# Kernel optimization log

Hardware: AMD Instinct MI355X
Metric: run time of the kernel (lower is better)

The kernel has to match this reference:

```python
import jax, jax.numpy as jnp
import numpy as np

LR = 0.1
N_HEADS = 4


def setup_inputs() -> dict:
    key = jax.random.key(0)
    ks = jax.random.split(key, 12)
    B, S, D, M, H = 2, 1024, 128, 512, 512
    s = 0.05
    return {
        "x": jax.random.normal(ks[0], (B, S, D), jnp.float32),
        "memory": jax.random.normal(ks[1], (M, D), jnp.float32) * s,
        "w_q": jax.random.normal(ks[2], (D, D), jnp.float32) * s,
        "w_k": jax.random.normal(ks[3], (D, D), jnp.float32) * s,
        "w_v": jax.random.normal(ks[4], (D, D), jnp.float32) * s,
        "b_q": jax.random.normal(ks[5], (D,), jnp.float32) * s,
        "b_k": jax.random.normal(ks[6], (D,), jnp.float32) * s,
        "b_v": jax.random.normal(ks[7], (D,), jnp.float32) * s,
        "w_o": jax.random.normal(ks[8], (D, D), jnp.float32) * s,
        "b_o": jax.random.normal(ks[9], (D,), jnp.float32) * s,
        "w_fc": jax.random.normal(ks[10], (H, D), jnp.float32) * s,
        "b_fc": jax.random.normal(ks[11], (H,), jnp.float32) * s,
    }


def reference(x, memory, w_q, w_k, w_v, b_q, b_k, b_v, w_o, b_o, w_fc, b_fc):
    B, S, D = x.shape
    M = memory.shape[0]
    hd = D // N_HEADS

    # --- LongTermMemory update (broadcast pairwise diff [B,S,M,D]) ---
    diff = x[:, :, None, :] - memory[None, None, :, :]          # [B,S,M,D]
    surprise = jnp.sqrt(jnp.sum(diff * diff, axis=-1, keepdims=True))  # [B,S,M,1]
    agg = jnp.mean(LR * surprise * diff, axis=(0, 1))           # [M,D]
    # torch does memory.data += agg (detached in-place update)
    mem = memory + jax.lax.stop_gradient(agg)                    # [M,D]

    # --- MultiheadAttention(query=x, key=mem, value=mem), batch_first ---
    # mem is identical across batch, so project once.
    q = (x @ w_q.T + b_q).reshape(B, S, N_HEADS, hd)
    k = (mem @ w_k.T + b_k).reshape(M, N_HEADS, hd)
    v = (mem @ w_v.T + b_v).reshape(M, N_HEADS, hd)
    scores = jnp.einsum('bshd,mhd->bhsm', q, k) / jnp.sqrt(jnp.asarray(hd, x.dtype))
    attn = jax.nn.softmax(scores, axis=-1)
    ctx = jnp.einsum('bhsm,mhd->bshd', attn, v).reshape(B, S, D)
    attn_out = ctx @ w_o.T + b_o                                 # [B,S,D]

    # --- Linear + ReLU ---
    return jax.nn.relu(attn_out @ w_fc.T + b_fc)                 # [B,S,hidden]
```

## Files before the change

### kernel.cpp

```cpp
#include <hip/hip_runtime.h>
#include <hip/hip_bf16.h>
#include <math.h>

#define SS 1024
#define MM 512
#define LRC (0.1f/2048.0f)
#define SCALE 0.17677669529663687f

typedef __attribute__((ext_vector_type(8))) short s8v;
typedef __attribute__((ext_vector_type(4))) float f32x4;
#define MFMA16(a, b, c) __builtin_amdgcn_mfma_f32_16x16x32_bf16(a, b, c, 0, 0, 0)

__device__ __forceinline__ unsigned short f2b(float f) {
  union { float f; unsigned int u; } v; v.f = f;
  return (unsigned short)((v.u + 0x7FFFu + ((v.u >> 16) & 1u)) >> 16);
}

__global__ __launch_bounds__(256) void k_prep(
    const float* __restrict__ x, const float* __restrict__ mem,
    const float* __restrict__ wq, const float* __restrict__ wk,
    const float* __restrict__ wv, const float* __restrict__ wo,
    const float* __restrict__ wfc,
    unsigned short* __restrict__ xbf, unsigned short* __restrict__ xT,
    float* __restrict__ xnorm, unsigned short* __restrict__ membf,
    float* __restrict__ mnorm,
    unsigned short* __restrict__ wqb, unsigned short* __restrict__ wkb,
    unsigned short* __restrict__ wvb, unsigned short* __restrict__ wob,
    unsigned short* __restrict__ wfcb) {
  const int t = threadIdx.x, bx = blockIdx.x;
  __shared__ float xl[64][132];
  if (bx < 32) {
    const int r0 = bx * 64;
    for (int i = t; i < 2048; i += 256) {
      int r = i >> 5, c4 = (i & 31) * 4;
      float4 v = *reinterpret_cast<const float4*>(&x[(r0 + r) * 128 + c4]);
      xl[r][c4] = v.x; xl[r][c4+1] = v.y; xl[r][c4+2] = v.z; xl[r][c4+3] = v.w;
      ushort4 u; u.x = f2b(v.x); u.y = f2b(v.y); u.z = f2b(v.z); u.w = f2b(v.w);
      *reinterpret_cast<ushort4*>(&xbf[(r0 + r) * 128 + c4]) = u;
    }
    __syncthreads();
    {
      int r = t >> 2, q = t & 3;
      float s = 0.f;
      #pragma unroll
      for (int j = 0; j < 32; ++j) { float v = xl[r][q * 32 + j]; s += v * v; }
      s += __shfl_xor(s, 1); s += __shfl_xor(s, 2);
      if (q == 0) xnorm[r0 + r] = s;
    }
    {
      int d = t >> 1, hh = t & 1;
      #pragma unroll
      for (int j4 = 0; j4 < 32; j4 += 4) {
        ushort4 u;
        u.x = f2b(xl[hh*32 + j4    ][d]);
        u.y = f2b(xl[hh*32 + j4 + 1][d]);
        u.z = f2b(xl[hh*32 + j4 + 2][d]);
        u.w = f2b(xl[hh*32 + j4 + 3][d]);
        *reinterpret_cast<ushort4*>(&xT[d * 2048 + r0 + hh*32 + j4]) = u;
      }
    }
  } else if (bx < 40) {
    const int r0 = (bx - 32) * 64;
    for (int i = t; i < 2048; i += 256) {
      int r = i >> 5, c4 = (i & 31) * 4;
      float4 v = *reinterpret_cast<const float4*>(&mem[(r0 + r) * 128 + c4]);
      xl[r][c4] = v.x; xl[r][c4+1] = v.y; xl[r][c4+2] = v.z; xl[r][c4+3] = v.w;
      ushort4 u; u.x = f2b(v.x); u.y = f2b(v.y); u.z = f2b(v.z); u.w = f2b(v.w);
      *reinterpret_cast<ushort4*>(&membf[(r0 + r) * 128 + c4]) = u;
    }
    __syncthreads();
    int r = t >> 2, q = t & 3;
    float s = 0.f;
    #pragma unroll
    for (int j = 0; j < 32; ++j) { float v = xl[r][q * 32 + j]; s += v * v; }
    s += __shfl_xor(s, 1); s += __shfl_xor(s, 2);
    if (q == 0) mnorm[r0 + r] = s;
  } else {
    const float* src; unsigned short* dst; int off = 0;
    if (bx == 40)      { src = wq;  dst = wqb; }
    else if (bx == 41) { src = wk;  dst = wkb; }
    else if (bx == 42) { src = wv;  dst = wvb; }
    else if (bx == 43) { src = wo;  dst = wob; }
    else               { src = wfc; dst = wfcb; off = (bx - 44) * 16384; }
    for (int i = t; i < 4096; i += 256) {
      float4 v = *reinterpret_cast<const float4*>(&src[off + i * 4]);
      ushort4 u; u.x = f2b(v.x); u.y = f2b(v.y); u.z = f2b(v.z); u.w = f2b(v.w);
      *reinterpret_cast<ushort4*>(&dst[off + i * 4]) = u;
    }
  }
}

__global__ __launch_bounds__(256) void k_surp(
    const unsigned short* __restrict__ xbf, const unsigned short* __restrict__ membf,
    const float* __restrict__ xnorm, const float* __restrict__ mnorm,
    unsigned short* __restrict__ STb) {
  const int t = threadIdx.x;
  const int bs0 = blockIdx.x * 64, m0 = blockIdx.y * 64;
  const int w = t >> 6, l = t & 63;
  const int kq = (l >> 4) * 8;
  const int arow = bs0 + w * 16 + (l & 15);
  f32x4 acc[4] = {};
  #pragma unroll
  for (int kc = 0; kc < 4; ++kc) {
    s8v a = *reinterpret_cast<const s8v*>(&xbf[arow * 128 + kc * 32 + kq]);
    #pragma unroll
    for (int mt = 0; mt < 4; ++mt) {
      s8v b = *reinterpret_cast<const s8v*>(&membf[(m0 + mt*16 + (l&15)) * 128 + kc*32 + kq]);
      acc[mt] = MFMA16(a, b, acc[mt]);
    }
  }
  const int r0 = bs0 + w * 16 + (l >> 4) * 4;
  float xn[4];
  #pragma unroll
  for (int i = 0; i < 4; ++i) xn[i] = xnorm[r0 + i];
  #pragma unroll
  for (int mt = 0; mt < 4; ++mt) {
    const int col = m0 + mt * 16 + (l & 15);
    const float mn = mnorm[col];
    ushort4 u;
    u.x = f2b(sqrtf(fmaxf(0.f, xn[0] + mn - 2.f * acc[mt][0])));
    u.y = f2b(sqrtf(fmaxf(0.f, xn[1] + mn - 2.f * acc[mt][1])));
    u.z = f2b(sqrtf(fmaxf(0.f, xn[2] + mn - 2.f * acc[mt][2])));
    u.w = f2b(sqrtf(fmaxf(0.f, xn[3] + mn - 2.f * acc[mt][3])));
    *reinterpret_cast<ushort4*>(&STb[col * 2048 + r0]) = u;
  }
}

__global__ __launch_bounds__(256) void k_qkv(
    const unsigned short* __restrict__ xbf, const unsigned short* __restrict__ STb,
    const unsigned short* __restrict__ xT, const float* __restrict__ mem,
    const unsigned short* __restrict__ wqb, const unsigned short* __restrict__ wkb,
    const unsigned short* __restrict__ wvb,
    const float* __restrict__ bq, const float* __restrict__ bk,
    const float* __restrict__ bv,
    unsigned short* __restrict__ qbf, unsigned short* __restrict__ kbf,
    unsigned short* __restrict__ vT) {
  __shared__ float Tld[16][132];
  __shared__ float srowl[16];
  __shared__ unsigned short mnl[16][136];
  const int t = threadIdx.x, bx = blockIdx.x;
  const int w = t >> 6, l = t & 63;
  const int kq = (l >> 4) * 8;
  const int r0l = (l >> 4) * 4;
  if (bx < 32) {
    const int s0 = bx * 64;
    const int arow = s0 + w * 16 + (l & 15);
    f32x4 acc[8] = {};
    #pragma unroll
    for (int kc = 0; kc < 4; ++kc) {
      s8v a = *reinterpret_cast<const s8v*>(&xbf[arow * 128 + kc * 32 + kq]);
      #pragma unroll
      for (int nt = 0; nt < 8; ++nt) {
        s8v b = *reinterpret_cast<const s8v*>(&wqb[(nt*16 + (l&15)) * 128 + kc*32 + kq]);
        acc[nt] = MFMA16(a, b, acc[nt]);
      }
    }
    const int r0 = s0 + w * 16 + r0l;
    #pragma unroll
    for (int nt = 0; nt < 8; ++nt) {
      const int col = nt * 16 + (l & 15);
      const float bb = bq[col];
      #pragma unroll
      for (int i = 0; i < 4; ++i)
        qbf[(r0 + i) * 128 + col] = f2b((acc[nt][i] + bb) * SCALE);
    }
  } else {
    const bool isv = bx >= 64;
    const int m0 = (isv ? (bx - 64) : (bx - 32)) * 16;
    f32x4 acc[2] = {};
    float ssum = 0.f;
    const int arow = m0 + (l & 15);
    #pragma unroll 4
    for (int kk = 0; kk < 64; ++kk) {
      s8v a = *reinterpret_cast<const s8v*>(&STb[arow * 2048 + kk * 32 + kq]);
      #pragma unroll
      for (int j = 0; j < 8; ++j) {
        union { unsigned int u; float f; } cv;
        cv.u = ((unsigned int)(unsigned short)a[j]) << 16;
        ssum += cv.f;
      }
      #pragma unroll
      for (int nt = 0; nt < 2; ++nt) {
        s8v b = *reinterpret_cast<const s8v*>(&xT[(w*32 + nt*16 + (l&15)) * 2048 + kk*32 + kq]);
        acc[nt] = MFMA16(a, b, acc[nt]);
      }
    }
    ssum += __shfl_xor(ssum, 16); ssum += __shfl_xor(ssum, 32);
    if (w == 0 && l < 16) srowl[l] = ssum;
    #pragma unroll
    for (int nt = 0; nt < 2; ++nt) {
      const int col = w * 32 + nt * 16 + (l & 15);
      #pragma unroll
      for (int i = 0; i < 4; ++i) Tld[r0l + i][col] = acc[nt][i];
    }
    __syncthreads();
    #pragma unroll
    for (int i = 0; i < 8; ++i) {
      const int flat = t + 256 * i;
      const int r = flat >> 7, c = flat & 127;
      const float mv = mem[(m0 + r) * 128 + c];
      mnl[r][c] = f2b(mv + LRC * (Tld[r][c] - srowl[r] * mv));
    }
    __syncthreads();
    const unsigned short* W = isv ? wvb : wkb;
    const float* bias = isv ? bv : bk;
    f32x4 pacc[2] = {};
    #pragma unroll
    for (int kc = 0; kc < 4; ++kc) {
      s8v a = *reinterpret_cast<const s8v*>(&mnl[l & 15][kc * 32 + kq]);
      #pragma unroll
      for (int nt = 0; nt < 2; ++nt) {
        s8v b = *reinterpret_cast<const s8v*>(&W[(w*32 + nt*16 + (l&15)) * 128 + kc*32 + kq]);
        pacc[nt] = MFMA16(a, b, pacc[nt]);
      }
    }
    #pragma unroll
    for (int nt = 0; nt < 2; ++nt) {
      const int col = w * 32 + nt * 16 + (l & 15);
      const float bb = bias[col];
      if (!isv) {
        #pragma unroll
        for (int i = 0; i < 4; ++i)
          kbf[(m0 + r0l + i) * 128 + col] = f2b(pacc[nt][i] + bb);
      } else {
        ushort4 u;
        u.x = f2b(pacc[nt][0] + bb); u.y = f2b(pacc[nt][1] + bb);
        u.z = f2b(pacc[nt][2] + bb); u.w = f2b(pacc[nt][3] + bb);
        *reinterpret_cast<ushort4*>(&vT[col * 512 + m0 + r0l]) = u;
      }
    }
  }
}

__global__ __launch_bounds__(256) void k_scores(
    const unsigned short* __restrict__ qbf, const unsigned short* __restrict__ kbf,
    unsigned short* __restrict__ P) {
  const int t = threadIdx.x;
  const int sB = blockIdx.x * 64;
  const int bh = blockIdx.y;
  const int b = bh >> 2, h = bh & 3;
  const int w = t >> 6, l = t & 63;
  const int kq = (l >> 4) * 8;
  const int arow = b * SS + sB + w * 16 + (l & 15);
  const s8v a = *reinterpret_cast<const s8v*>(&qbf[arow * 128 + h * 32 + kq]);
  f32x4 acc[32];
  #pragma unroll
  for (int mt = 0; mt < 32; ++mt) acc[mt] = f32x4{0.f, 0.f, 0.f, 0.f};
  #pragma unroll
  for (int mt = 0; mt < 32; ++mt) {
    s8v b2 = *reinterpret_cast<const s8v*>(&kbf[(mt*16 + (l&15)) * 128 + h*32 + kq]);
    acc[mt] = MFMA16(a, b2, acc[mt]);
  }
  const int prow0 = bh * SS + sB + w * 16 + (l >> 4) * 4;
  #pragma unroll
  for (int i = 0; i < 4; ++i) {
    float mx = acc[0][i];
    #pragma unroll
    for (int mt = 1; mt < 32; ++mt) mx = fmaxf(mx, acc[mt][i]);
    mx = fmaxf(mx, __shfl_xor(mx, 1));
    mx = fmaxf(mx, __shfl_xor(mx, 2));
    mx = fmaxf(mx, __shfl_xor(mx, 4));
    mx = fmaxf(mx, __shfl_xor(mx, 8));
    float sm = 0.f;
    #pragma unroll
    for (int mt = 0; mt < 32; ++mt) {
      float e = __expf(acc[mt][i] - mx); acc[mt][i] = e; sm += e;
    }
    sm += __shfl_xor(sm, 1); sm += __shfl_xor(sm, 2);
    sm += __shfl_xor(sm, 4); sm += __shfl_xor(sm, 8);
    const float inv = 1.f / sm;
    #pragma unroll
    for (int mt = 0; mt < 32; ++mt)
      P[(prow0 + i) * 512 + mt * 16 + (l & 15)] = f2b(acc[mt][i] * inv);
  }
}

__global__ __launch_bounds__(256) void k_pv(
    const unsigned short* __restrict__ P, const unsigned short* __restrict__ vT,
    unsigned short* __restrict__ ctx) {
  const int t = threadIdx.x;
  const int sB = blockIdx.x * 64;
  const int bh = blockIdx.y;
  const int b = bh >> 2, h = bh & 3;
  const int w = t >> 6, l = t & 63;
  const int kq = (l >> 4) * 8;
  const int arow = bh * SS + sB + w * 16 + (l & 15);
  f32x4 acc[2] = {};
  #pragma unroll 4
  for (int kk = 0; kk < 16; ++kk) {
    s8v a = *reinterpret_cast<const s8v*>(&P[arow * 512 + kk * 32 + kq]);
    #pragma unroll
    for (int nt = 0; nt < 2; ++nt) {
      s8v b2 = *reinterpret_cast<const s8v*>(&vT[(h*32 + nt*16 + (l&15)) * 512 + kk*32 + kq]);
      acc[nt] = MFMA16(a, b2, acc[nt]);
    }
  }
  const int r0 = b * SS + sB + w * 16 + (l >> 4) * 4;
  #pragma unroll
  for (int nt = 0; nt < 2; ++nt) {
    const int col = h * 32 + nt * 16 + (l & 15);
    #pragma unroll
    for (int i = 0; i < 4; ++i)
      ctx[(r0 + i) * 128 + col] = f2b(acc[nt][i]);
  }
}

__global__ __launch_bounds__(256) void k_wofc(
    const unsigned short* __restrict__ ctx, const unsigned short* __restrict__ wob,
    const float* __restrict__ bo, const unsigned short* __restrict__ wfcb,
    const float* __restrict__ bfc, float* __restrict__ out) {
  __shared__ unsigned short al[32][136];
  const int t = threadIdx.x;
  const int rows0 = blockIdx.x * 32;
  const int w = t >> 6, l = t & 63;
  const int rt = w >> 1, ch = w & 1;
  const int kq = (l >> 4) * 8;
  {
    const int arow = rows0 + rt * 16 + (l & 15);
    f32x4 acc[4] = {};
    #pragma unroll
    for (int kc = 0; kc < 4; ++kc) {
      s8v a = *reinterpret_cast<const s8v*>(&ctx[arow * 128 + kc * 32 + kq]);
      #pragma unroll
      for (int nt = 0; nt < 4; ++nt) {
        s8v b2 = *reinterpret_cast<const s8v*>(&wob[(ch*64 + nt*16 + (l&15)) * 128 + kc*32 + kq]);
        acc[nt] = MFMA16(a, b2, acc[nt]);
      }
    }
    const int rl0 = rt * 16 + (l >> 4) * 4;
    #pragma unroll
    for (int nt = 0; nt < 4; ++nt) {
      const int col = ch * 64 + nt * 16 + (l & 15);
      const float bb = bo[col];
      #pragma unroll
      for (int i = 0; i < 4; ++i) al[rl0 + i][col] = f2b(acc[nt][i] + bb);
    }
  }
  __syncthreads();
  {
    f32x4 acc[16] = {};
    #pragma unroll
    for (int kc = 0; kc < 4; ++kc) {
      s8v a = *reinterpret_cast<const s8v*>(&al[rt * 16 + (l & 15)][kc * 32 + kq]);
      #pragma unroll
      for (int nt = 0; nt < 16; ++nt) {
        s8v b2 = *reinterpret_cast<const s8v*>(&wfcb[(ch*256 + nt*16 + (l&15)) * 128 + kc*32 + kq]);
        acc[nt] = MFMA16(a, b2, acc[nt]);
      }
    }
    const int r0 = rows0 + rt * 16 + (l >> 4) * 4;
    #pragma unroll
    for (int nt = 0; nt < 16; ++nt) {
      const int col = ch * 256 + nt * 16 + (l & 15);
      const float bb = bfc[col];
      #pragma unroll
      for (int i = 0; i < 4; ++i)
        out[(r0 + i) * 512 + col] = fmaxf(acc[nt][i] + bb, 0.f);
    }
  }
}

extern "C" void kernel_launch(void* const* d_in, const int* in_sizes, int n_in,
                              void* d_out, int out_size, void* d_ws, size_t ws_size,
                              hipStream_t stream) {
  const float* x    = (const float*)d_in[0];
  const float* mem  = (const float*)d_in[1];
  const float* w_q  = (const float*)d_in[2];
  const float* w_k  = (const float*)d_in[3];
  const float* w_v  = (const float*)d_in[4];
  const float* b_q  = (const float*)d_in[5];
  const float* b_k  = (const float*)d_in[6];
  const float* b_v  = (const float*)d_in[7];
  const float* w_o  = (const float*)d_in[8];
  const float* b_o  = (const float*)d_in[9];
  const float* w_fc = (const float*)d_in[10];
  const float* b_fc = (const float*)d_in[11];
  float* out = (float*)d_out;

  char* base = (char*)d_ws;
  unsigned short* P     = (unsigned short*)(base);
  unsigned short* STb   = (unsigned short*)(base + 8388608);
  unsigned short* xbf   = (unsigned short*)(base + 10485760);
  unsigned short* xT    = (unsigned short*)(base + 11010048);
  unsigned short* qbf   = (unsigned short*)(base + 11534336);
  unsigned short* ctx   = (unsigned short*)(base + 12058624);
  unsigned short* kbf   = (unsigned short*)(base + 12582912);
  unsigned short* vT    = (unsigned short*)(base + 12713984);
  unsigned short* membf = (unsigned short*)(base + 12845056);
  unsigned short* wfcb  = (unsigned short*)(base + 12976128);
  unsigned short* wqb   = (unsigned short*)(base + 13107200);
  unsigned short* wkb   = (unsigned short*)(base + 13139968);
  unsigned short* wvb   = (unsigned short*)(base + 13172736);
  unsigned short* wob   = (unsigned short*)(base + 13205504);
  float* xnorm          = (float*)(base + 13238272);
  float* mnorm          = (float*)(base + 13246464);

  k_prep<<<48, 256, 0, stream>>>(x, mem, w_q, w_k, w_v, w_o, w_fc,
                                 xbf, xT, xnorm, membf, mnorm,
                                 wqb, wkb, wvb, wob, wfcb);
  k_surp<<<dim3(32, 8), 256, 0, stream>>>(xbf, membf, xnorm, mnorm, STb);
  k_qkv<<<96, 256, 0, stream>>>(xbf, STb, xT, mem, wqb, wkb, wvb,
                                b_q, b_k, b_v, qbf, kbf, vT);
  k_scores<<<dim3(16, 8), 256, 0, stream>>>(qbf, kbf, P);
  k_pv<<<dim3(16, 8), 256, 0, stream>>>(P, vT, ctx);
  k_wofc<<<64, 256, 0, stream>>>(ctx, wob, b_o, wfcb, b_fc, out);
}
```

Baseline: 72.31 us.

## Fuse six kernels into three: prep+surprise+Q, K/V update, attention+output MLP

Merges prep, surprise distance and Q projection into one kernel whose blocks each convert their own x and memory tiles in shared memory. K and V projections now share one block per memory row tile instead of two. Scores, softmax, PV, output projection and FC run in one kernel, with the probability matrix and context kept in shared memory rather than written to and re-read from global memory. This removes three launches and large intermediate global buffers, at the cost of redundant conversions of x and memory per block and fewer blocks (32) in the K/V stage.

```diff
diff --git a/kernel.cpp b/kernel.cpp
--- a/kernel.cpp
+++ b/kernel.cpp
@@ -16,194 +16,204 @@
   return (unsigned short)((v.u + 0x7FFFu + ((v.u >> 16) & 1u)) >> 16);
 }
 
-__global__ __launch_bounds__(256) void k_prep(
+__global__ __launch_bounds__(256) void k_p1(
     const float* __restrict__ x, const float* __restrict__ mem,
     const float* __restrict__ wq, const float* __restrict__ wk,
     const float* __restrict__ wv, const float* __restrict__ wo,
-    const float* __restrict__ wfc,
-    unsigned short* __restrict__ xbf, unsigned short* __restrict__ xT,
-    float* __restrict__ xnorm, unsigned short* __restrict__ membf,
-    float* __restrict__ mnorm,
-    unsigned short* __restrict__ wqb, unsigned short* __restrict__ wkb,
-    unsigned short* __restrict__ wvb, unsigned short* __restrict__ wob,
-    unsigned short* __restrict__ wfcb) {
-  const int t = threadIdx.x, bx = blockIdx.x;
-  __shared__ float xl[64][132];
-  if (bx < 32) {
-    const int r0 = bx * 64;
-    for (int i = t; i < 2048; i += 256) {
-      int r = i >> 5, c4 = (i & 31) * 4;
-      float4 v = *reinterpret_cast<const float4*>(&x[(r0 + r) * 128 + c4]);
-      xl[r][c4] = v.x; xl[r][c4+1] = v.y; xl[r][c4+2] = v.z; xl[r][c4+3] = v.w;
-      ushort4 u; u.x = f2b(v.x); u.y = f2b(v.y); u.z = f2b(v.z); u.w = f2b(v.w);
-      *reinterpret_cast<ushort4*>(&xbf[(r0 + r) * 128 + c4]) = u;
-    }
-    __syncthreads();
-    {
-      int r = t >> 2, q = t & 3;
-      float s = 0.f;
-      #pragma unroll
-      for (int j = 0; j < 32; ++j) { float v = xl[r][q * 32 + j]; s += v * v; }
-      s += __shfl_xor(s, 1); s += __shfl_xor(s, 2);
-      if (q == 0) xnorm[r0 + r] = s;
-    }
-    {
-      int d = t >> 1, hh = t & 1;
-      #pragma unroll
-      for (int j4 = 0; j4 < 32; j4 += 4) {
-        ushort4 u;
-        u.x = f2b(xl[hh*32 + j4    ][d]);
-        u.y = f2b(xl[hh*32 + j4 + 1][d]);
-        u.z = f2b(xl[hh*32 + j4 + 2][d]);
-        u.w = f2b(xl[hh*32 + j4 + 3][d]);
-        *reinterpret_cast<ushort4*>(&xT[d * 2048 + r0 + hh*32 + j4]) = u;
-      }
-    }
-  } else if (bx < 40) {
-    const int r0 = (bx - 32) * 64;
-    for (int i = t; i < 2048; i += 256) {
-      int r = i >> 5, c4 = (i & 31) * 4;
-      float4 v = *reinterpret_cast<const float4*>(&mem[(r0 + r) * 128 + c4]);
-      xl[r][c4] = v.x; xl[r][c4+1] = v.y; xl[r][c4+2] = v.z; xl[r][c4+3] = v.w;
-      ushort4 u; u.x = f2b(v.x); u.y = f2b(v.y); u.z = f2b(v.z); u.w = f2b(v.w);
-      *reinterpret_cast<ushort4*>(&membf[(r0 + r) * 128 + c4]) = u;
-    }
-    __syncthreads();
-    int r = t >> 2, q = t & 3;
-    float s = 0.f;
-    #pragma unroll
-    for (int j = 0; j < 32; ++j) { float v = xl[r][q * 32 + j]; s += v * v; }
-    s += __shfl_xor(s, 1); s += __shfl_xor(s, 2);
-    if (q == 0) mnorm[r0 + r] = s;
-  } else {
-    const float* src; unsigned short* dst; int off = 0;
-    if (bx == 40)      { src = wq;  dst = wqb; }
-    else if (bx == 41) { src = wk;  dst = wkb; }
-    else if (bx == 42) { src = wv;  dst = wvb; }
-    else if (bx == 43) { src = wo;  dst = wob; }
-    else               { src = wfc; dst = wfcb; off = (bx - 44) * 16384; }
-    for (int i = t; i < 4096; i += 256) {
-      float4 v = *reinterpret_cast<const float4*>(&src[off + i * 4]);
-      ushort4 u; u.x = f2b(v.x); u.y = f2b(v.y); u.z = f2b(v.z); u.w = f2b(v.w);
-      *reinterpret_cast<ushort4*>(&dst[off + i * 4]) = u;
-    }
-  }
-}
-
-__global__ __launch_bounds__(256) void k_surp(
-    const unsigned short* __restrict__ xbf, const unsigned short* __restrict__ membf,
-    const float* __restrict__ xnorm, const float* __restrict__ mnorm,
-    unsigned short* __restrict__ STb) {
-  const int t = threadIdx.x;
-  const int bs0 = blockIdx.x * 64, m0 = blockIdx.y * 64;
-  const int w = t >> 6, l = t & 63;
-  const int kq = (l >> 4) * 8;
-  const int arow = bs0 + w * 16 + (l & 15);
-  f32x4 acc[4] = {};
-  #pragma unroll
-  for (int kc = 0; kc < 4; ++kc) {
-    s8v a = *reinterpret_cast<const s8v*>(&xbf[arow * 128 + kc * 32 + kq]);
-    #pragma unroll
-    for (int mt = 0; mt < 4; ++mt) {
-      s8v b = *reinterpret_cast<const s8v*>(&membf[(m0 + mt*16 + (l&15)) * 128 + kc*32 + kq]);
-      acc[mt] = MFMA16(a, b, acc[mt]);
-    }
-  }
-  const int r0 = bs0 + w * 16 + (l >> 4) * 4;
-  float xn[4];
-  #pragma unroll
-  for (int i = 0; i < 4; ++i) xn[i] = xnorm[r0 + i];
-  #pragma unroll
-  for (int mt = 0; mt < 4; ++mt) {
-    const int col = m0 + mt * 16 + (l & 15);
-    const float mn = mnorm[col];
-    ushort4 u;
-    u.x = f2b(sqrtf(fmaxf(0.f, xn[0] + mn - 2.f * acc[mt][0])));
-    u.y = f2b(sqrtf(fmaxf(0.f, xn[1] + mn - 2.f * acc[mt][1])));
-    u.z = f2b(sqrtf(fmaxf(0.f, xn[2] + mn - 2.f * acc[mt][2])));
-    u.w = f2b(sqrtf(fmaxf(0.f, xn[3] + mn - 2.f * acc[mt][3])));
-    *reinterpret_cast<ushort4*>(&STb[col * 2048 + r0]) = u;
-  }
-}
-
-__global__ __launch_bounds__(256) void k_qkv(
-    const unsigned short* __restrict__ xbf, const unsigned short* __restrict__ STb,
-    const unsigned short* __restrict__ xT, const float* __restrict__ mem,
-    const unsigned short* __restrict__ wqb, const unsigned short* __restrict__ wkb,
-    const unsigned short* __restrict__ wvb,
-    const float* __restrict__ bq, const float* __restrict__ bk,
-    const float* __restrict__ bv,
-    unsigned short* __restrict__ qbf, unsigned short* __restrict__ kbf,
-    unsigned short* __restrict__ vT) {
-  __shared__ float Tld[16][132];
-  __shared__ float srowl[16];
-  __shared__ unsigned short mnl[16][136];
+    const float* __restrict__ wfc, const float* __restrict__ bq,
+    unsigned short* __restrict__ STb, unsigned short* __restrict__ xT,
+    unsigned short* __restrict__ qbf,
+    unsigned short* __restrict__ wkb, unsigned short* __restrict__ wvb,
+    unsigned short* __restrict__ wob, unsigned short* __restrict__ wfcb) {
+  __shared__ alignas(16) char smem[69376];
   const int t = threadIdx.x, bx = blockIdx.x;
   const int w = t >> 6, l = t & 63;
   const int kq = (l >> 4) * 8;
   const int r0l = (l >> 4) * 4;
-  if (bx < 32) {
-    const int s0 = bx * 64;
-    const int arow = s0 + w * 16 + (l & 15);
+
+  if (bx < 256) {
+    float (*xl)[132]          = reinterpret_cast<float (*)[132]>(smem);
+    unsigned short (*xb)[136] = reinterpret_cast<unsigned short (*)[136]>(smem + 33792);
+    unsigned short (*mb)[136] = reinterpret_cast<unsigned short (*)[136]>(smem + 51200);
+    float* xn                 = reinterpret_cast<float*>(smem + 68608);
+    float* mn                 = reinterpret_cast<float*>(smem + 68864);
+    const int bs0 = (bx & 31) * 64, m0 = (bx >> 5) * 64;
+
+    for (int i = t; i < 2048; i += 256) {
+      int r = i >> 5, c4 = (i & 31) * 4;
+      float4 v = *reinterpret_cast<const float4*>(&x[(bs0 + r) * 128 + c4]);
+      xl[r][c4] = v.x; xl[r][c4+1] = v.y; xl[r][c4+2] = v.z; xl[r][c4+3] = v.w;
+      ushort4 u; u.x = f2b(v.x); u.y = f2b(v.y); u.z = f2b(v.z); u.w = f2b(v.w);
+      *reinterpret_cast<ushort4*>(&xb[r][c4]) = u;
+    }
+    __syncthreads();
+    {
+      int r = t >> 2, q = t & 3;
+      float s = 0.f;
+      #pragma unroll
+      for (int j = 0; j < 32; ++j) { float v = xl[r][q * 32 + j]; s += v * v; }
+      s += __shfl_xor(s, 1); s += __shfl_xor(s, 2);
+      if (q == 0) xn[r] = s;
+    }
+    if ((bx >> 5) == 0) {
+      int d = t >> 1, hh = t & 1;
+      #pragma unroll
+      for (int j4 = 0; j4 < 32; j4 += 4) {
+        ushort4 u;
+        u.x = xb[hh*32 + j4    ][d];
+        u.y = xb[hh*32 + j4 + 1][d];
+        u.z = xb[hh*32 + j4 + 2][d];
+        u.w = xb[hh*32 + j4 + 3][d];
+        *reinterpret_cast<ushort4*>(&xT[d * 2048 + bs0 + hh*32 + j4]) = u;
+      }
+    }
+    __syncthreads();
+    for (int i = t; i < 2048; i += 256) {
+      int r = i >> 5, c4 = (i & 31) * 4;
+      float4 v = *reinterpret_cast<const float4*>(&mem[(m0 + r) * 128 + c4]);
+      xl[r][c4] = v.x; xl[r][c4+1] = v.y; xl[r][c4+2] = v.z; xl[r][c4+3] = v.w;
+      ushort4 u; u.x = f2b(v.x); u.y = f2b(v.y); u.z = f2b(v.z); u.w = f2b(v.w);
+      *reinterpret_cast<ushort4*>(&mb[r][c4]) = u;
+    }
+    __syncthreads();
+    {
+      int r = t >> 2, q = t & 3;
+      float s = 0.f;
+      #pragma unroll
+      for (int j = 0; j < 32; ++j) { float v = xl[r][q * 32 + j]; s += v * v; }
+      s += __shfl_xor(s, 1); s += __shfl_xor(s, 2);
+      if (q == 0) mn[r] = s;
+    }
+    __syncthreads();
+    f32x4 acc[4] = {};
+    #pragma unroll
+    for (int kc = 0; kc < 4; ++kc) {
+      s8v a = *reinterpret_cast<const s8v*>(&xb[w*16 + (l&15)][kc*32 + kq]);
+      #pragma unroll
+      for (int mt = 0; mt < 4; ++mt) {
+        s8v b = *reinterpret_cast<const s8v*>(&mb[mt*16 + (l&15)][kc*32 + kq]);
+        acc[mt] = MFMA16(a, b, acc[mt]);
+      }
+    }
+    const int r0g = bs0 + w * 16 + r0l;
+    float xnr[4];
+    #pragma unroll
+    for (int i = 0; i < 4; ++i) xnr[i] = xn[w*16 + r0l + i];
+    #pragma unroll
+    for (int mt = 0; mt < 4; ++mt) {
+      const int coll = mt * 16 + (l & 15);
+      const float mnv = mn[coll];
+      ushort4 u;
+      u.x = f2b(sqrtf(fmaxf(0.f, xnr[0] + mnv - 2.f * acc[mt][0])));
+      u.y = f2b(sqrtf(fmaxf(0.f, xnr[1] + mnv - 2.f * acc[mt][1])));
+      u.z = f2b(sqrtf(fmaxf(0.f, xnr[2] + mnv - 2.f * acc[mt][2])));
+      u.w = f2b(sqrtf(fmaxf(0.f, xnr[3] + mnv - 2.f * acc[mt][3])));
+      *reinterpret_cast<ushort4*>(&STb[(m0 + coll) * 2048 + r0g]) = u;
+    }
+  } else if (bx < 288) {
+    unsigned short (*xb)[136]  = reinterpret_cast<unsigned short (*)[136]>(smem);
+    unsigned short (*wql)[136] = reinterpret_cast<unsigned short (*)[136]>(smem + 17408);
+    const int s0 = (bx - 256) * 64;
+    for (int i = t; i < 2048; i += 256) {
+      int r = i >> 5, c4 = (i & 31) * 4;
+      float4 v = *reinterpret_cast<const float4*>(&x[(s0 + r) * 128 + c4]);
+      ushort4 u; u.x = f2b(v.x); u.y = f2b(v.y); u.z = f2b(v.z); u.w = f2b(v.w);
+      *reinterpret_cast<ushort4*>(&xb[r][c4]) = u;
+    }
+    for (int i = t; i < 4096; i += 256) {
+      int r = i >> 5, c4 = (i & 31) * 4;
+      float4 v = *reinterpret_cast<const float4*>(&wq[r * 128 + c4]);
+      ushort4 u; u.x = f2b(v.x); u.y = f2b(v.y); u.z = f2b(v.z); u.w = f2b(v.w);
+      *reinterpret_cast<ushort4*>(&wql[r][c4]) = u;
+    }
+    __syncthreads();
     f32x4 acc[8] = {};
     #pragma unroll
     for (int kc = 0; kc < 4; ++kc) {
-      s8v a = *reinterpret_cast<const s8v*>(&xbf[arow * 128 + kc * 32 + kq]);
+      s8v a = *reinterpret_cast<const s8v*>(&xb[w*16 + (l&15)][kc*32 + kq]);
       #pragma unroll
       for (int nt = 0; nt < 8; ++nt) {
-        s8v b = *reinterpret_cast<const s8v*>(&wqb[(nt*16 + (l&15)) * 128 + kc*32 + kq]);
+        s8v b = *reinterpret_cast<const s8v*>(&wql[nt*16 + (l&15)][kc*32 + kq]);
         acc[nt] = MFMA16(a, b, acc[nt]);
       }
     }
-    const int r0 = s0 + w * 16 + r0l;
+    const int r0g = s0 + w * 16 + r0l;
     #pragma unroll
     for (int nt = 0; nt < 8; ++nt) {
       const int col = nt * 16 + (l & 15);
       const float bb = bq[col];
       #pragma unroll
       for (int i = 0; i < 4; ++i)
-        qbf[(r0 + i) * 128 + col] = f2b((acc[nt][i] + bb) * SCALE);
+        qbf[(r0g + i) * 128 + col] = f2b((acc[nt][i] + bb) * SCALE);
     }
   } else {
-    const bool isv = bx >= 64;
-    const int m0 = (isv ? (bx - 64) : (bx - 32)) * 16;
-    f32x4 acc[2] = {};
-    float ssum = 0.f;
-    const int arow = m0 + (l & 15);
-    #pragma unroll 4
-    for (int kk = 0; kk < 64; ++kk) {
-      s8v a = *reinterpret_cast<const s8v*>(&STb[arow * 2048 + kk * 32 + kq]);
-      #pragma unroll
-      for (int j = 0; j < 8; ++j) {
-        union { unsigned int u; float f; } cv;
-        cv.u = ((unsigned int)(unsigned short)a[j]) << 16;
-        ssum += cv.f;
-      }
-      #pragma unroll
-      for (int nt = 0; nt < 2; ++nt) {
-        s8v b = *reinterpret_cast<const s8v*>(&xT[(w*32 + nt*16 + (l&15)) * 2048 + kk*32 + kq]);
-        acc[nt] = MFMA16(a, b, acc[nt]);
-      }
-    }
-    ssum += __shfl_xor(ssum, 16); ssum += __shfl_xor(ssum, 32);
-    if (w == 0 && l < 16) srowl[l] = ssum;
+    const float* src; unsigned short* dst; int off = 0;
+    if (bx == 288)      { src = wk;  dst = wkb; }
+    else if (bx == 289) { src = wv;  dst = wvb; }
+    else if (bx == 290) { src = wo;  dst = wob; }
+    else                { src = wfc; dst = wfcb; off = (bx - 291) * 16384; }
+    for (int i = t; i < 4096; i += 256) {
+      float4 v = *reinterpret_cast<const float4*>(&src[off + i * 4]);
+      ushort4 u; u.x = f2b(v.x); u.y = f2b(v.y); u.z = f2b(v.z); u.w = f2b(v.w);
+      *reinterpret_cast<ushort4*>(&dst[off + i * 4]) = u;
+    }
+  }
+}
+
+__global__ __launch_bounds__(256) void k_p2(
+    const unsigned short* __restrict__ STb, const unsigned short* __restrict__ xT,
+    const float* __restrict__ mem,
+    const unsigned short* __restrict__ wkb, const unsigned short* __restrict__ wvb,
+    const float* __restrict__ bk, const float* __restrict__ bv,
+    unsigned short* __restrict__ kbf, unsigned short* __restrict__ vT) {
+  __shared__ float Tld[16][132];
+  __shared__ float srowl[16];
+  __shared__ unsigned short mnl[16][136];
+  const int t = threadIdx.x;
+  const int w = t >> 6, l = t & 63;
+  const int kq = (l >> 4) * 8;
+  const int r0l = (l >> 4) * 4;
+  const int m0 = blockIdx.x * 16;
+
+  f32x4 acc[2] = {};
+  float ssum = 0.f;
+  const int arow = m0 + (l & 15);
+  #pragma unroll 4
+  for (int kk = 0; kk < 64; ++kk) {
+    s8v a = *reinterpret_cast<const s8v*>(&STb[arow * 2048 + kk * 32 + kq]);
+    #pragma unroll
+    for (int j = 0; j < 8; ++j) {
+      union { unsigned int u; float f; } cv;
+      cv.u = ((unsigned int)(unsigned short)a[j]) << 16;
+      ssum += cv.f;
+    }
     #pragma unroll
     for (int nt = 0; nt < 2; ++nt) {
-      const int col = w * 32 + nt * 16 + (l & 15);
-      #pragma unroll
-      for (int i = 0; i < 4; ++i) Tld[r0l + i][col] = acc[nt][i];
-    }
-    __syncthreads();
-    #pragma unroll
-    for (int i = 0; i < 8; ++i) {
-      const int flat = t + 256 * i;
-      const int r = flat >> 7, c = flat & 127;
-      const float mv = mem[(m0 + r) * 128 + c];
-      mnl[r][c] = f2b(mv + LRC * (Tld[r][c] - srowl[r] * mv));
-    }
-    __syncthreads();
-    const unsigned short* W = isv ? wvb : wkb;
-    const float* bias = isv ? bv : bk;
+      s8v b = *reinterpret_cast<const s8v*>(&xT[(w*32 + nt*16 + (l&15)) * 2048 + kk*32 + kq]);
+      acc[nt] = MFMA16(a, b, acc[nt]);
+    }
+  }
+  ssum += __shfl_xor(ssum, 16); ssum += __shfl_xor(ssum, 32);
+  if (w == 0 && l < 16) srowl[l] = ssum;
+  #pragma unroll
+  for (int nt = 0; nt < 2; ++nt) {
+    const int col = w * 32 + nt * 16 + (l & 15);
+    #pragma unroll
+    for (int i = 0; i < 4; ++i) Tld[r0l + i][col] = acc[nt][i];
+  }
+  __syncthreads();
+  #pragma unroll
+  for (int i = 0; i < 8; ++i) {
+    const int flat = t + 256 * i;
+    const int r = flat >> 7, c = flat & 127;
+    const float mv = mem[(m0 + r) * 128 + c];
+    mnl[r][c] = f2b(mv + LRC * (Tld[r][c] - srowl[r] * mv));
+  }
+  __syncthreads();
+  #pragma unroll
+  for (int p = 0; p < 2; ++p) {
+    const unsigned short* W = p ? wvb : wkb;
+    const float* bias = p ? bv : bk;
     f32x4 pacc[2] = {};
     #pragma unroll
     for (int kc = 0; kc < 4; ++kc) {
@@ -218,7 +228,7 @@
     for (int nt = 0; nt < 2; ++nt) {
       const int col = w * 32 + nt * 16 + (l & 15);
       const float bb = bias[col];
-      if (!isv) {
+      if (p == 0) {
         #pragma unroll
         for (int i = 0; i < 4; ++i)
           kbf[(m0 + r0l + i) * 128 + col] = f2b(pacc[nt][i] + bb);
@@ -232,130 +242,113 @@
   }
 }
 
-__global__ __launch_bounds__(256) void k_scores(
+__global__ __launch_bounds__(256) void k_p3(
     const unsigned short* __restrict__ qbf, const unsigned short* __restrict__ kbf,
-    unsigned short* __restrict__ P) {
+    const unsigned short* __restrict__ vT, const unsigned short* __restrict__ wob,
+    const unsigned short* __restrict__ wfcb, const float* __restrict__ bo,
+    const float* __restrict__ bfc, float* __restrict__ out) {
+  __shared__ alignas(16) char smem[75264];
+  unsigned short (*Pl)[520] = reinterpret_cast<unsigned short (*)[520]>(smem);
+  unsigned short (*cl)[136] = reinterpret_cast<unsigned short (*)[136]>(smem + 66560);
+  unsigned short (*al)[136] = reinterpret_cast<unsigned short (*)[136]>(smem + 70912);
   const int t = threadIdx.x;
-  const int sB = blockIdx.x * 64;
-  const int bh = blockIdx.y;
-  const int b = bh >> 2, h = bh & 3;
   const int w = t >> 6, l = t & 63;
   const int kq = (l >> 4) * 8;
-  const int arow = b * SS + sB + w * 16 + (l & 15);
-  const s8v a = *reinterpret_cast<const s8v*>(&qbf[arow * 128 + h * 32 + kq]);
-  f32x4 acc[32];
-  #pragma unroll
-  for (int mt = 0; mt < 32; ++mt) acc[mt] = f32x4{0.f, 0.f, 0.f, 0.f};
-  #pragma unroll
-  for (int mt = 0; mt < 32; ++mt) {
-    s8v b2 = *reinterpret_cast<const s8v*>(&kbf[(mt*16 + (l&15)) * 128 + h*32 + kq]);
-    acc[mt] = MFMA16(a, b2, acc[mt]);
-  }
-  const int prow0 = bh * SS + sB + w * 16 + (l >> 4) * 4;
-  #pragma unroll
-  for (int i = 0; i < 4; ++i) {
-    float mx = acc[0][i];
-    #pragma unroll
-    for (int mt = 1; mt < 32; ++mt) mx = fmaxf(mx, acc[mt][i]);
-    mx = fmaxf(mx, __shfl_xor(mx, 1));
-    mx = fmaxf(mx, __shfl_xor(mx, 2));
-    mx = fmaxf(mx, __shfl_xor(mx, 4));
-    mx = fmaxf(mx, __shfl_xor(mx, 8));
-    float sm = 0.f;
+  const int r0l = (l >> 4) * 4;
+  const int r0 = blockIdx.x * 16;
+
+  {
+    const int h = w;
+    const s8v a = *reinterpret_cast<const s8v*>(&qbf[(r0 + (l & 15)) * 128 + h * 32 + kq]);
+    f32x4 acc[32];
+    #pragma unroll
+    for (int mt = 0; mt < 32; ++mt) acc[mt] = f32x4{0.f, 0.f, 0.f, 0.f};
     #pragma unroll
     for (int mt = 0; mt < 32; ++mt) {
-      float e = __expf(acc[mt][i] - mx); acc[mt][i] = e; sm += e;
-    }
-    sm += __shfl_xor(sm, 1); sm += __shfl_xor(sm, 2);
-    sm += __shfl_xor(sm, 4); sm += __shfl_xor(sm, 8);
-    const float inv = 1.f / sm;
-    #pragma unroll
-    for (int mt = 0; mt < 32; ++mt)
-      P[(prow0 + i) * 512 + mt * 16 + (l & 15)] = f2b(acc[mt][i] * inv);
-  }
-}
-
-__global__ __launch_bounds__(256) void k_pv(
-    const unsigned short* __restrict__ P, const unsigned short* __restrict__ vT,
-    unsigned short* __restrict__ ctx) {
-  const int t = threadIdx.x;
-  const int sB = blockIdx.x * 64;
-  const int bh = blockIdx.y;
-  const int b = bh >> 2, h = bh & 3;
-  const int w = t >> 6, l = t & 63;
-  const int kq = (l >> 4) * 8;
-  const int arow = bh * SS + sB + w * 16 + (l & 15);
-  f32x4 acc[2] = {};
-  #pragma unroll 4
-  for (int kk = 0; kk < 16; ++kk) {
-    s8v a = *reinterpret_cast<const s8v*>(&P[arow * 512 + kk * 32 + kq]);
+      s8v b2 = *reinterpret_cast<const s8v*>(&kbf[(mt*16 + (l&15)) * 128 + h*32 + kq]);
+      acc[mt] = MFMA16(a, b2, acc[mt]);
+    }
+    #pragma unroll
+    for (int i = 0; i < 4; ++i) {
+      float mx = acc[0][i];
+      #pragma unroll
+      for (int mt = 1; mt < 32; ++mt) mx = fmaxf(mx, acc[mt][i]);
+      mx = fmaxf(mx, __shfl_xor(mx, 1));
+      mx = fmaxf(mx, __shfl_xor(mx, 2));
+      mx = fmaxf(mx, __shfl_xor(mx, 4));
+      mx = fmaxf(mx, __shfl_xor(mx, 8));
+      float sm = 0.f;
+      #pragma unroll
+      for (int mt = 0; mt < 32; ++mt) {
+        float e = __expf(acc[mt][i] - mx); acc[mt][i] = e; sm += e;
+      }
+      sm += __shfl_xor(sm, 1); sm += __shfl_xor(sm, 2);
+      sm += __shfl_xor(sm, 4); sm += __shfl_xor(sm, 8);
+      const float inv = 1.f / sm;
+      #pragma unroll
+      for (int mt = 0; mt < 32; ++mt)
+        Pl[h * 16 + r0l + i][mt * 16 + (l & 15)] = f2b(acc[mt][i] * inv);
+    }
+  }
+  __syncthreads();
+  {
+    const int h = w;
+    f32x4 acc[2] = {};
+    #pragma unroll 4
+    for (int kk = 0; kk < 16; ++kk) {
+      s8v a = *reinterpret_cast<const s8v*>(&Pl[h * 16 + (l & 15)][kk * 32 + kq]);
+      #pragma unroll
+      for (int nt = 0; nt < 2; ++nt) {
+        s8v b2 = *reinterpret_cast<const s8v*>(&vT[(h*32 + nt*16 + (l&15)) * 512 + kk*32 + kq]);
+        acc[nt] = MFMA16(a, b2, acc[nt]);
+      }
+    }
     #pragma unroll
     for (int nt = 0; nt < 2; ++nt) {
-      s8v b2 = *reinterpret_cast<const s8v*>(&vT[(h*32 + nt*16 + (l&15)) * 512 + kk*32 + kq]);
-      acc[nt] = MFMA16(a, b2, acc[nt]);
-    }
-  }
-  const int r0 = b * SS + sB + w * 16 + (l >> 4) * 4;
-  #pragma unroll
-  for (int nt = 0; nt < 2; ++nt) {
-    const int col = h * 32 + nt * 16 + (l & 15);
-    #pragma unroll
-    for (int i = 0; i < 4; ++i)
-      ctx[(r0 + i) * 128 + col] = f2b(acc[nt][i]);
-  }
-}
-
-__global__ __launch_bounds__(256) void k_wofc(
-    const unsigned short* __restrict__ ctx, const unsigned short* __restrict__ wob,
-    const float* __restrict__ bo, const unsigned short* __restrict__ wfcb,
-    const float* __restrict__ bfc, float* __restrict__ out) {
-  __shared__ unsigned short al[32][136];
-  const int t = threadIdx.x;
-  const int rows0 = blockIdx.x * 32;
-  const int w = t >> 6, l = t & 63;
-  const int rt = w >> 1, ch = w & 1;
-  const int kq = (l >> 4) * 8;
+      const int col = h * 32 + nt * 16 + (l & 15);
+      #pragma unroll
+      for (int i = 0; i < 4; ++i) cl[r0l + i][col] = f2b(acc[nt][i]);
+    }
+  }
+  __syncthreads();
   {
-    const int arow = rows0 + rt * 16 + (l & 15);
-    f32x4 acc[4] = {};
-    #pragma unroll
-    for (int kc = 0; kc < 4; ++kc) {
-      s8v a = *reinterpret_cast<const s8v*>(&ctx[arow * 128 + kc * 32 + kq]);
-      #pragma unroll
-      for (int nt = 0; nt < 4; ++nt) {
-        s8v b2 = *reinterpret_cast<const s8v*>(&wob[(ch*64 + nt*16 + (l&15)) * 128 + kc*32 + kq]);
+    f32x4 acc[2] = {};
+    #pragma unroll
+    for (int kc = 0; kc < 4; ++kc) {
+      s8v a = *reinterpret_cast<const s8v*>(&cl[l & 15][kc * 32 + kq]);
+      #pragma unroll
+      for (int nt = 0; nt < 2; ++nt) {
+        s8v b2 = *reinterpret_cast<const s8v*>(&wob[(w*32 + nt*16 + (l&15)) * 128 + kc*32 + kq]);
         acc[nt] = MFMA16(a, b2, acc[nt]);
       }
     }
-    const int rl0 = rt * 16 + (l >> 4) * 4;
-    #pragma unroll
-    for (int nt = 0; nt < 4; ++nt) {
-      const int col = ch * 64 + nt * 16 + (l & 15);
+    #pragma unroll
+    for (int nt = 0; nt < 2; ++nt) {
+      const int col = w * 32 + nt * 16 + (l & 15);
       const float bb = bo[col];
       #pragma unroll
-      for (int i = 0; i < 4; ++i) al[rl0 + i][col] = f2b(acc[nt][i] + bb);
+      for (int i = 0; i < 4; ++i) al[r0l + i][col] = f2b(acc[nt][i] + bb);
     }
   }
   __syncthreads();
   {
-    f32x4 acc[16] = {};
-    #pragma unroll
-    for (int kc = 0; kc < 4; ++kc) {
-      s8v a = *reinterpret_cast<const s8v*>(&al[rt * 16 + (l & 15)][kc * 32 + kq]);
-      #pragma unroll
-      for (int nt = 0; nt < 16; ++nt) {
-        s8v b2 = *reinterpret_cast<const s8v*>(&wfcb[(ch*256 + nt*16 + (l&15)) * 128 + kc*32 + kq]);
+    f32x4 acc[8] = {};
+    #pragma unroll
+    for (int kc = 0; kc < 4; ++kc) {
+      s8v a = *reinterpret_cast<const s8v*>(&al[l & 15][kc * 32 + kq]);
+      #pragma unroll
+      for (int nt = 0; nt < 8; ++nt) {
+        s8v b2 = *reinterpret_cast<const s8v*>(&wfcb[(w*128 + nt*16 + (l&15)) * 128 + kc*32 + kq]);
         acc[nt] = MFMA16(a, b2, acc[nt]);
       }
     }
-    const int r0 = rows0 + rt * 16 + (l >> 4) * 4;
-    #pragma unroll
-    for (int nt = 0; nt < 16; ++nt) {
-      const int col = ch * 256 + nt * 16 + (l & 15);
+    #pragma unroll
+    for (int nt = 0; nt < 8; ++nt) {
+      const int col = w * 128 + nt * 16 + (l & 15);
       const float bb = bfc[col];
       #pragma unroll
       for (int i = 0; i < 4; ++i)
-        out[(r0 + i) * 512 + col] = fmaxf(acc[nt][i] + bb, 0.f);
+        out[(r0 + r0l + i) * 512 + col] = fmaxf(acc[nt][i] + bb, 0.f);
     }
   }
 }
@@ -378,30 +371,18 @@
   float* out = (float*)d_out;
 
   char* base = (char*)d_ws;
-  unsigned short* P     = (unsigned short*)(base);
-  unsigned short* STb   = (unsigned short*)(base + 8388608);
-  unsigned short* xbf   = (unsigned short*)(base + 10485760);
-  unsigned short* xT    = (unsigned short*)(base + 11010048);
-  unsigned short* qbf   = (unsigned short*)(base + 11534336);
-  unsigned short* ctx   = (unsigned short*)(base + 12058624);
-  unsigned short* kbf   = (unsigned short*)(base + 12582912);
-  unsigned short* vT    = (unsigned short*)(base + 12713984);
-  unsigned short* membf = (unsigned short*)(base + 12845056);
-  unsigned short* wfcb  = (unsigned short*)(base + 12976128);
-  unsigned short* wqb   = (unsigned short*)(base + 13107200);
-  unsigned short* wkb   = (unsigned short*)(base + 13139968);
-  unsigned short* wvb   = (unsigned short*)(base + 13172736);
-  unsigned short* wob   = (unsigned short*)(base + 13205504);
-  float* xnorm          = (float*)(base + 13238272);
-  float* mnorm          = (float*)(base + 13246464);
-
-  k_prep<<<48, 256, 0, stream>>>(x, mem, w_q, w_k, w_v, w_o, w_fc,
-                                 xbf, xT, xnorm, membf, mnorm,
-                                 wqb, wkb, wvb, wob, wfcb);
-  k_surp<<<dim3(32, 8), 256, 0, stream>>>(xbf, membf, xnorm, mnorm, STb);
-  k_qkv<<<96, 256, 0, stream>>>(xbf, STb, xT, mem, wqb, wkb, wvb,
-                                b_q, b_k, b_v, qbf, kbf, vT);
-  k_scores<<<dim3(16, 8), 256, 0, stream>>>(qbf, kbf, P);
-  k_pv<<<dim3(16, 8), 256, 0, stream>>>(P, vT, ctx);
-  k_wofc<<<64, 256, 0, stream>>>(ctx, wob, b_o, wfcb, b_fc, out);
-}
+  unsigned short* STb  = (unsigned short*)(base);
+  unsigned short* xT   = (unsigned short*)(base + 2097152);
+  unsigned short* qbf  = (unsigned short*)(base + 2621440);
+  unsigned short* kbf  = (unsigned short*)(base + 3145728);
+  unsigned short* vT   = (unsigned short*)(base + 3276800);
+  unsigned short* wkb  = (unsigned short*)(base + 3407872);
+  unsigned short* wvb  = (unsigned short*)(base + 3440640);
+  unsigned short* wob  = (unsigned short*)(base + 3473408);
+  unsigned short* wfcb = (unsigned short*)(base + 3506176);
+
+  k_p1<<<295, 256, 0, stream>>>(x, mem, w_q, w_k, w_v, w_o, w_fc, b_q,
+                                STb, xT, qbf, wkb, wvb, wob, wfcb);
+  k_p2<<<32, 256, 0, stream>>>(STb, xT, mem, wkb, wvb, b_k, b_v, kbf, vT);
+  k_p3<<<128, 256, 0, stream>>>(qbf, kbf, vT, wob, wfcb, b_o, b_fc, out);
+}
```

After: 58.91 us, median of 3. 18.5% less time.
